# Performance work log

Measured on AMD Instinct MI355X. Metric: run time of the kernel, lower is better.

## Reference

```python
import jax, jax.numpy as jnp
import numpy as np

BETA = 0.25
EPS = 1e-12  # torch F.normalize eps


def _normalize(x):
    n = jnp.linalg.norm(x, axis=-1, keepdims=True)
    return x / jnp.maximum(n, EPS)


def setup_inputs() -> dict:
    key = jax.random.key(0)
    k1, k2 = jax.random.split(key)
    B, S, D, NE = 16, 2048, 512, 8192
    z = jax.random.normal(k1, (B, S, D), dtype=jnp.float32)
    emb = jax.random.normal(k2, (NE, D), dtype=jnp.float32)
    return {"z": z, "emb": emb}


def reference(z, emb):
    B, S, D = z.shape
    n_e = emb.shape[0]
    zf = z.reshape(-1, D)                      # [N, D]
    zn = _normalize(zf)
    embn = _normalize(emb)                     # [n_e, D]
    # squared euclidean distances: [N, n_e]
    d = (jnp.sum(zn * zn, axis=1, keepdims=True)
         + jnp.sum(embn * embn, axis=1)
         - 2.0 * jnp.matmul(zn, embn.T))
    idx = jnp.argmin(d, axis=1)                # [N]
    z_q = emb[idx].reshape(z.shape)            # raw codebook lookup (NOT normalized)
    # commitment / codebook loss on normalized vectors
    z_q_n = _normalize(z_q)
    z_n = _normalize(z)
    sg = jax.lax.stop_gradient
    loss = (jnp.mean((z_q_n - sg(z_n)) ** 2)
            + BETA * jnp.mean((sg(z_q_n) - z_n) ** 2))
    # straight-through estimator, then normalize
    z_q_st = z + sg(z_q - z)
    z_q_st = _normalize(z_q_st)
    # perplexity via usage counts (equivalent to mean of one-hots)
    N = zf.shape[0]
    counts = jnp.zeros((n_e,), dtype=z.dtype).at[idx].add(1.0)
    e_mean = counts / N
    perplexity = jnp.exp(-jnp.sum(e_mean * jnp.log(e_mean + 1e-10)))
    return loss, z_q_st, idx, perplexity
```

## Files before the change

kernel.cpp:

```cpp
#include <hip/hip_runtime.h>
#include <float.h>
#include <math.h>

#define DIM 512
#define EPSN 1e-12f

typedef _Float16 f16x8 __attribute__((ext_vector_type(8)));
typedef float f32x4 __attribute__((ext_vector_type(4)));

__device__ inline void gll16(const void* g, void* l) {
  __builtin_amdgcn_global_load_lds(
      (__attribute__((address_space(1))) void*)g,
      (__attribute__((address_space(3))) void*)l, 16, 0, 0);
}

__device__ inline float wave_sum(float v) {
#pragma unroll
  for (int o = 32; o > 0; o >>= 1) v += __shfl_xor(v, o, 64);
  return v;
}

__global__ __launch_bounds__(256) void emb_norm_kernel(
    const float* __restrict__ emb, float2* __restrict__ eepair) {
  int row = blockIdx.x * 4 + (threadIdx.x >> 6);
  int lane = threadIdx.x & 63;
  const float* p = emb + (size_t)row * DIM;
  float x[8];
  float ss = 0.f;
#pragma unroll
  for (int i = 0; i < 8; ++i) { x[i] = p[i * 64 + lane]; ss += x[i] * x[i]; }
  ss = wave_sum(ss);
  float d = fmaxf(sqrtf(ss), EPSN);
  float ee = 0.f;
#pragma unroll
  for (int i = 0; i < 8; ++i) { float y = x[i] / d; ee += y * y; }
  ee = wave_sum(ee);
  if (lane == 0) eepair[row] = make_float2(ee, 1.0f / d);
}

__global__ __launch_bounds__(256) void z_norm_kernel(
    const float* __restrict__ z, float* __restrict__ zinv) {
  int row = blockIdx.x * 4 + (threadIdx.x >> 6);
  int lane = threadIdx.x & 63;
  const float* p = z + (size_t)row * DIM;
  float ss = 0.f;
#pragma unroll
  for (int i = 0; i < 8; ++i) { float v = p[i * 64 + lane]; ss += v * v; }
  ss = wave_sum(ss);
  if (lane == 0) zinv[row] = 1.0f / fmaxf(sqrtf(ss), EPSN);
}

__global__ __launch_bounds__(256) void emb_split_kernel(
    const float* __restrict__ emb, _Float16* __restrict__ swz) {
  int g = blockIdx.x * 256 + threadIdx.x;
  int lane = g & 63;
  int kc = (g >> 6) & 15;
  int t = g >> 10;
  int code = t * 16 + (lane & 15);
  int k0 = kc * 32 + (lane >> 4) * 8;
  const float* src = emb + (size_t)code * DIM + k0;
  float4 a = *(const float4*)src;
  float4 b = *(const float4*)(src + 4);
  float v[8] = {a.x, a.y, a.z, a.w, b.x, b.y, b.z, b.w};
  f16x8 h, l;
#pragma unroll
  for (int k = 0; k < 8; ++k) {
    _Float16 hh = (_Float16)v[k];
    h[k] = hh;
    l[k] = (_Float16)(v[k] - (float)hh);
  }
  size_t cbase = ((size_t)(t * 16 + kc) * 2) * 512;
  *(f16x8*)&swz[cbase + lane * 8] = h;
  *(f16x8*)&swz[cbase + 512 + lane * 8] = l;
}

#define MFMA16(A, B, C) __builtin_amdgcn_mfma_f32_16x16x32_f16(A, B, C, 0, 0, 0)

__global__ __launch_bounds__(256, 1) void dist_argmin_kernel(
    const float* __restrict__ z, const _Float16* __restrict__ swz,
    const float2* __restrict__ eepair, const float* __restrict__ zinv,
    int ne, int* __restrict__ idxw, float* __restrict__ counts,
    float* __restrict__ out_idx) {
  __shared__ _Float16 B[2][32768];

  const int tid = threadIdx.x;
  const int wave = tid >> 6;
  const int lane = tid & 63;
  const int col = lane & 15;
  const int quad = lane >> 4;
  const int r0 = blockIdx.x * 128 + wave * 32;

  f16x8 Ah[2][16], Al[2][16];
#pragma unroll
  for (int rb = 0; rb < 2; ++rb) {
    const float* zp = z + (size_t)(r0 + rb * 16 + col) * DIM + quad * 8;
#pragma unroll
    for (int kc = 0; kc < 16; ++kc) {
      float4 a = *(const float4*)(zp + kc * 32);
      float4 b = *(const float4*)(zp + kc * 32 + 4);
      float v[8] = {a.x, a.y, a.z, a.w, b.x, b.y, b.z, b.w};
#pragma unroll
      for (int k = 0; k < 8; ++k) {
        _Float16 h = (_Float16)v[k];
        Ah[rb][kc][k] = h;
        Al[rb][kc][k] = (_Float16)(v[k] - (float)h);
      }
    }
  }

  float zr[2][4];
#pragma unroll
  for (int rb = 0; rb < 2; ++rb)
#pragma unroll
    for (int i = 0; i < 4; ++i)
      zr[rb][i] = zinv[r0 + rb * 16 + quad * 4 + i];

  float best[2][4] = {{FLT_MAX, FLT_MAX, FLT_MAX, FLT_MAX},
                      {FLT_MAX, FLT_MAX, FLT_MAX, FLT_MAX}};
  int bidx[2][4] = {{0, 0, 0, 0}, {0, 0, 0, 0}};

  const int ntiles = ne / 32;

  {
    const _Float16* g0 = swz + (size_t)(wave * 16) * 512 + lane * 8;
    _Float16* l0 = &B[0][(wave * 16) * 512 + lane * 8];
#pragma unroll
    for (int i = 0; i < 16; ++i)
      gll16(g0 + i * 512, l0 + i * 512);
  }
  __syncthreads();

  for (int t = 0; t < ntiles; ++t) {
    const int buf = t & 1;

    if (t + 1 < ntiles) {
      const _Float16* g0 =
          swz + ((size_t)(t + 1) * 64 + wave * 16) * 512 + lane * 8;
      _Float16* l0 = &B[buf ^ 1][(wave * 16) * 512 + lane * 8];
#pragma unroll
      for (int i = 0; i < 16; ++i)
        gll16(g0 + i * 512, l0 + i * 512);
    }

#pragma unroll
    for (int s = 0; s < 2; ++s) {
      const int n0 = (t * 2 + s) * 16;
      float2 ep = eepair[n0 + col];

      f32x4 acc[2][3];
#pragma unroll
      for (int rb = 0; rb < 2; ++rb)
#pragma unroll
        for (int a = 0; a < 3; ++a) acc[rb][a] = (f32x4){0.f, 0.f, 0.f, 0.f};

      const _Float16* bp = &B[buf][(s * 32) * 512 + lane * 8];
#pragma unroll
      for (int kc = 0; kc < 16; ++kc) {
        f16x8 bh = *(const f16x8*)(bp + (kc * 2) * 512);
        f16x8 bl = *(const f16x8*)(bp + (kc * 2 + 1) * 512);
        acc[0][0] = MFMA16(Ah[0][kc], bh, acc[0][0]);
        acc[1][0] = MFMA16(Ah[1][kc], bh, acc[1][0]);
        acc[0][1] = MFMA16(Al[0][kc], bh, acc[0][1]);
        acc[1][1] = MFMA16(Al[1][kc], bh, acc[1][1]);
        acc[0][2] = MFMA16(Ah[0][kc], bl, acc[0][2]);
        acc[1][2] = MFMA16(Ah[1][kc], bl, acc[1][2]);
      }

      float w2 = 2.0f * ep.y;
      int j = n0 + col;
#pragma unroll
      for (int rb = 0; rb < 2; ++rb)
#pragma unroll
        for (int i = 0; i < 4; ++i) {
          float d = acc[rb][0][i] + acc[rb][1][i] + acc[rb][2][i];
          float sc = ep.x - w2 * zr[rb][i] * d;
          if (sc < best[rb][i]) { best[rb][i] = sc; bidx[rb][i] = j; }
        }
    }
    __syncthreads();
  }

#pragma unroll
  for (int rb = 0; rb < 2; ++rb)
#pragma unroll
    for (int i = 0; i < 4; ++i) {
      float bs = best[rb][i];
      int bj = bidx[rb][i];
#pragma unroll
      for (int off = 1; off < 16; off <<= 1) {
        float os = __shfl_xor(bs, off, 64);
        int oi = __shfl_xor(bj, off, 64);
        if (os < bs || (os == bs && oi < bj)) { bs = os; bj = oi; }
      }
      if (col == 0) {
        int row = r0 + rb * 16 + quad * 4 + i;
        idxw[row] = bj;
        out_idx[row] = (float)bj;
        atomicAdd(&counts[bj], 1.0f);
      }
    }
}

__global__ __launch_bounds__(256) void finalize_rows_kernel(
    const float* __restrict__ z, const float* __restrict__ emb,
    const int* __restrict__ idxw, const float* __restrict__ zinv,
    float* __restrict__ out_zq, float* __restrict__ lpart) {
  __shared__ float red[4];
  int row = blockIdx.x * 4 + (threadIdx.x >> 6);
  int lane = threadIdx.x & 63;
  int j = idxw[row];
  const float* zp = z + (size_t)row * DIM;
  const float* qp = emb + (size_t)j * DIM;
  float zl[8], ql[8], tl[8];
  float st = 0.f, sq = 0.f;
#pragma unroll
  for (int i = 0; i < 8; ++i) {
    int k = i * 64 + lane;
    float zv = zp[k], qv = qp[k];
    float t = zv + (qv - zv);
    zl[i] = zv; ql[i] = qv; tl[i] = t;
    st += t * t;
    sq += qv * qv;
  }
  st = wave_sum(st);
  sq = wave_sum(sq);
  float dt = fmaxf(sqrtf(st), EPSN);
  float dq = fmaxf(sqrtf(sq), EPSN);
  float zi = zinv[row];
  float lp = 0.f;
#pragma unroll
  for (int i = 0; i < 8; ++i) {
    int k = i * 64 + lane;
    out_zq[(size_t)row * DIM + k] = tl[i] / dt;
    float e = ql[i] / dq - zl[i] * zi;
    lp += e * e;
  }
  lp = wave_sum(lp);
  if (lane == 0) red[threadIdx.x >> 6] = lp;
  __syncthreads();
  if (threadIdx.x == 0) lpart[blockIdx.x] = red[0] + red[1] + red[2] + red[3];
}

__global__ __launch_bounds__(256) void scalars_kernel(
    const float* __restrict__ counts, const float* __restrict__ lpart,
    int ne, int nblk, float inv_n, float inv_total,
    float* __restrict__ out_loss, float* __restrict__ out_perp) {
  __shared__ float red[8];
  int tid = threadIdx.x;
  float s = 0.f;
  for (int jj = tid; jj < ne; jj += 256) {
    float p = counts[jj] * inv_n;
    s += p * logf(p + 1e-10f);
  }
  float l = 0.f;
  for (int jj = tid; jj < nblk; jj += 256) l += lpart[jj];
  s = wave_sum(s);
  l = wave_sum(l);
  if ((tid & 63) == 0) { red[tid >> 6] = s; red[4 + (tid >> 6)] = l; }
  __syncthreads();
  if (tid == 0) {
    float t = red[0] + red[1] + red[2] + red[3];
    float lt = red[4] + red[5] + red[6] + red[7];
    *out_perp = expf(-t);
    *out_loss = 1.25f * lt * inv_total;
  }
}

extern "C" void kernel_launch(void* const* d_in, const int* in_sizes, int n_in,
                              void* d_out, int out_size, void* d_ws, size_t ws_size,
                              hipStream_t stream) {
  const float* z = (const float*)d_in[0];
  const float* emb = (const float*)d_in[1];
  float* out = (float*)d_out;
  float* ws = (float*)d_ws;

  const int nrows = in_sizes[0] / DIM;
  const int ne = in_sizes[1] / DIM;
  const int nfin = nrows / 4;

  float2* eepair = (float2*)ws;
  float* zinv = ws + 2 * ne;
  int* idxw = (int*)(ws + 2 * ne + nrows);
  float* counts = ws + 2 * ne + 2 * nrows;
  float* lpart = counts + ne;
  _Float16* swz = (_Float16*)(lpart + nfin);

  float* out_zq = out + 1;
  float* out_idx = out + 1 + (size_t)nrows * DIM;
  float* out_perp = out + (size_t)out_size - 1;

  hipMemsetAsync(counts, 0, ne * sizeof(float), stream);
  emb_norm_kernel<<<ne / 4, 256, 0, stream>>>(emb, eepair);
  z_norm_kernel<<<nrows / 4, 256, 0, stream>>>(z, zinv);
  emb_split_kernel<<<ne * 64 / 256, 256, 0, stream>>>(emb, swz);
  dist_argmin_kernel<<<nrows / 128, 256, 0, stream>>>(z, swz, eepair, zinv, ne,
                                                      idxw, counts, out_idx);
  finalize_rows_kernel<<<nfin, 256, 0, stream>>>(z, emb, idxw, zinv,
                                                 out_zq, lpart);
  scalars_kernel<<<1, 256, 0, stream>>>(counts, lpart, ne, nfin,
                                        1.0f / (float)nrows,
                                        1.0f / (float)((size_t)nrows * DIM),
                                        out, out_perp);
}
```

Baseline: 1.111 ms.

## Deepen codebook prefetch to 4-stage LDS ring with staggered tile order

Replaces the double-buffered 32-code tile loop with a 4-buffer ring of 16-code tiles, keeping three tiles of global-to-LDS loads in flight. Waits use explicit vmcnt counts and a single barrier per tile. The eepair norms now come through LDS instead of direct global loads. Each block starts at a different codebook offset to spread L2 traffic, with a tie-break on index added to keep argmin deterministic. MFMA sections get raised wave priority. This adds hand-tuned waitcnt logic that depends on the exact number of issued loads.

```diff
diff --git a/kernel.cpp b/kernel.cpp
--- a/kernel.cpp
+++ b/kernel.cpp
@@ -81,7 +81,8 @@
     const float2* __restrict__ eepair, const float* __restrict__ zinv,
     int ne, int* __restrict__ idxw, float* __restrict__ counts,
     float* __restrict__ out_idx) {
-  __shared__ _Float16 B[2][32768];
+  __shared__ __attribute__((aligned(16))) _Float16 Bb[4][16384];
+  __shared__ __attribute__((aligned(16))) float Bep[4][1024];
 
   const int tid = threadIdx.x;
   const int wave = tid >> 6;
@@ -119,65 +120,76 @@
                       {FLT_MAX, FLT_MAX, FLT_MAX, FLT_MAX}};
   int bidx[2][4] = {{0, 0, 0, 0}, {0, 0, 0, 0}};
 
-  const int ntiles = ne / 32;
-
-  {
-    const _Float16* g0 = swz + (size_t)(wave * 16) * 512 + lane * 8;
-    _Float16* l0 = &B[0][(wave * 16) * 512 + lane * 8];
-#pragma unroll
-    for (int i = 0; i < 16; ++i)
-      gll16(g0 + i * 512, l0 + i * 512);
-  }
-  __syncthreads();
+  const int ntiles = ne / 16;
+  const int off = (blockIdx.x & 7) * (ntiles >> 3);
+
+  auto issue = [&](int t) {
+    const int g = (t + off) & (ntiles - 1);
+    const int buf = t & 3;
+    const _Float16* gb =
+        swz + (size_t)g * 16384 + (wave * 8) * 512 + lane * 8;
+    _Float16* lb = &Bb[buf][(wave * 8) * 512 + lane * 8];
+#pragma unroll
+    for (int i = 0; i < 8; ++i) gll16(gb + i * 512, lb + i * 512);
+    const float* ge = (const float*)eepair + (size_t)g * 32 + (lane & 7) * 4;
+    gll16(ge, &Bep[buf][wave * 256 + lane * 4]);
+  };
+
+  issue(0);
+  issue(1);
+  issue(2);
 
   for (int t = 0; t < ntiles; ++t) {
-    const int buf = t & 1;
-
-    if (t + 1 < ntiles) {
-      const _Float16* g0 =
-          swz + ((size_t)(t + 1) * 64 + wave * 16) * 512 + lane * 8;
-      _Float16* l0 = &B[buf ^ 1][(wave * 16) * 512 + lane * 8];
-#pragma unroll
-      for (int i = 0; i < 16; ++i)
-        gll16(g0 + i * 512, l0 + i * 512);
+    if (t < ntiles - 2)
+      asm volatile("s_waitcnt vmcnt(18)" ::: "memory");
+    else if (t == ntiles - 2)
+      asm volatile("s_waitcnt vmcnt(9)" ::: "memory");
+    else
+      asm volatile("s_waitcnt vmcnt(0)" ::: "memory");
+    __builtin_amdgcn_s_barrier();
+    __builtin_amdgcn_sched_barrier(0);
+
+    if (t + 3 < ntiles) issue(t + 3);
+
+    const int buf = t & 3;
+    const int g = (t + off) & (ntiles - 1);
+    float2 ep = *(const float2*)&Bep[buf][wave * 256 + col * 2];
+
+    f32x4 acc[2][3];
+#pragma unroll
+    for (int rb = 0; rb < 2; ++rb)
+#pragma unroll
+      for (int a = 0; a < 3; ++a) acc[rb][a] = (f32x4){0.f, 0.f, 0.f, 0.f};
+
+    const _Float16* bp = &Bb[buf][lane * 8];
+    __builtin_amdgcn_s_setprio(1);
+#pragma unroll
+    for (int kc = 0; kc < 16; ++kc) {
+      f16x8 bh = *(const f16x8*)(bp + (kc * 2) * 512);
+      f16x8 bl = *(const f16x8*)(bp + (kc * 2 + 1) * 512);
+      acc[0][0] = MFMA16(Ah[0][kc], bh, acc[0][0]);
+      acc[1][0] = MFMA16(Ah[1][kc], bh, acc[1][0]);
+      acc[0][1] = MFMA16(Al[0][kc], bh, acc[0][1]);
+      acc[1][1] = MFMA16(Al[1][kc], bh, acc[1][1]);
+      acc[0][2] = MFMA16(Ah[0][kc], bl, acc[0][2]);
+      acc[1][2] = MFMA16(Ah[1][kc], bl, acc[1][2]);
     }
-
-#pragma unroll
-    for (int s = 0; s < 2; ++s) {
-      const int n0 = (t * 2 + s) * 16;
-      float2 ep = eepair[n0 + col];
-
-      f32x4 acc[2][3];
-#pragma unroll
-      for (int rb = 0; rb < 2; ++rb)
-#pragma unroll
-        for (int a = 0; a < 3; ++a) acc[rb][a] = (f32x4){0.f, 0.f, 0.f, 0.f};
-
-      const _Float16* bp = &B[buf][(s * 32) * 512 + lane * 8];
-#pragma unroll
-      for (int kc = 0; kc < 16; ++kc) {
-        f16x8 bh = *(const f16x8*)(bp + (kc * 2) * 512);
-        f16x8 bl = *(const f16x8*)(bp + (kc * 2 + 1) * 512);
-        acc[0][0] = MFMA16(Ah[0][kc], bh, acc[0][0]);
-        acc[1][0] = MFMA16(Ah[1][kc], bh, acc[1][0]);
-        acc[0][1] = MFMA16(Al[0][kc], bh, acc[0][1]);
-        acc[1][1] = MFMA16(Al[1][kc], bh, acc[1][1]);
-        acc[0][2] = MFMA16(Ah[0][kc], bl, acc[0][2]);
-        acc[1][2] = MFMA16(Ah[1][kc], bl, acc[1][2]);
+    __builtin_amdgcn_s_setprio(0);
+
+    float w2 = 2.0f * ep.y;
+    int j = g * 16 + col;
+#pragma unroll
+    for (int rb = 0; rb < 2; ++rb)
+#pragma unroll
+      for (int i = 0; i < 4; ++i) {
+        float d = acc[rb][0][i] + acc[rb][1][i] + acc[rb][2][i];
+        float sc = ep.x - w2 * zr[rb][i] * d;
+        if (sc < best[rb][i] ||
+            (sc == best[rb][i] && j < bidx[rb][i])) {
+          best[rb][i] = sc;
+          bidx[rb][i] = j;
+        }
       }
-
-      float w2 = 2.0f * ep.y;
-      int j = n0 + col;
-#pragma unroll
-      for (int rb = 0; rb < 2; ++rb)
-#pragma unroll
-        for (int i = 0; i < 4; ++i) {
-          float d = acc[rb][0][i] + acc[rb][1][i] + acc[rb][2][i];
-          float sc = ep.x - w2 * zr[rb][i] * d;
-          if (sc < best[rb][i]) { best[rb][i] = sc; bidx[rb][i] = j; }
-        }
-    }
-    __syncthreads();
   }
 
 #pragma unroll
@@ -187,9 +199,9 @@
       float bs = best[rb][i];
       int bj = bidx[rb][i];
 #pragma unroll
-      for (int off = 1; off < 16; off <<= 1) {
-        float os = __shfl_xor(bs, off, 64);
-        int oi = __shfl_xor(bj, off, 64);
+      for (int offm = 1; offm < 16; offm <<= 1) {
+        float os = __shfl_xor(bs, offm, 64);
+        int oi = __shfl_xor(bj, offm, 64);
         if (os < bs || (os == bs && oi < bj)) { bs = os; bj = oi; }
       }
       if (col == 0) {
```

Result: slower. 1.277 ms (+14.9%).
